# Optimization experiments

Measured on AMD Instinct MI355X. Metric: run time of the kernel, lower is better.

The kernel has to match this reference:

```python
import jax, jax.numpy as jnp
import numpy as np

B, S, QD = 1, 2048, 3072          # batch, seq, query_dim
H, D = 24, 128                    # heads, head_dim
INNER = H * D                     # 3072
MLP = 4 * QD                      # mlp_hidden_dim = 12288
EPS = 1e-5


def setup_inputs() -> dict:
    key = jax.random.key(0)
    k0, k1, k2 = jax.random.split(key, 3)
    hidden_states = jax.random.normal(k0, (B, S, QD), dtype=jnp.float32)
    # RoPE tables (non-neox / interleaved), [S, D/2]
    pos = jnp.arange(S, dtype=jnp.float32)
    inv_freq = 1.0 / (10000.0 ** (jnp.arange(0, D, 2, dtype=jnp.float32) / D))
    ang = pos[:, None] * inv_freq[None, :]
    cos, sin = jnp.cos(ang), jnp.sin(ang)
    # learned params
    W_qkv_mlp = jax.random.normal(k1, (QD, 3 * INNER + 2 * MLP), dtype=jnp.float32) * 0.02
    norm_q_w = jnp.ones((D,), dtype=jnp.float32)
    norm_k_w = jnp.ones((D,), dtype=jnp.float32)
    W_out = jax.random.normal(k2, (INNER + MLP, QD), dtype=jnp.float32) * 0.02
    b_out = jnp.zeros((QD,), dtype=jnp.float32)
    return {"hidden_states": hidden_states, "cos": cos, "sin": sin,
            "W_qkv_mlp": W_qkv_mlp, "norm_q_w": norm_q_w, "norm_k_w": norm_k_w,
            "W_out": W_out, "b_out": b_out}


def _rmsnorm(x, w, eps):
    return x * jax.lax.rsqrt(jnp.mean(x * x, axis=-1, keepdims=True) + eps) * w


def _rope_interleaved(x, cos, sin):
    # x: [B,S,H,D]; cos/sin: [S,D/2]; non-neox pairing (x[2i], x[2i+1]); fp32 math
    xf = x.astype(jnp.float32)
    x1, x2 = xf[..., 0::2], xf[..., 1::2]
    c = cos[None, :, None, :]
    s = sin[None, :, None, :]
    r1 = x1 * c - x2 * s
    r2 = x2 * c + x1 * s
    out = jnp.stack([r1, r2], axis=-1).reshape(x.shape)
    return out.astype(x.dtype)


def reference(hidden_states, cos, sin, W_qkv_mlp, norm_q_w, norm_k_w, W_out, b_out):
    # fused QKV + MLP input projection (no bias)
    h = hidden_states @ W_qkv_mlp                       # [B,S,3*INNER+2*MLP]
    qkv, mlp_hidden = jnp.split(h, [3 * INNER], axis=-1)
    q, k, v = jnp.split(qkv, 3, axis=-1)
    q = q.reshape(B, S, H, D)
    k = k.reshape(B, S, H, D)
    v = v.reshape(B, S, H, D)
    # per-head RMSNorm on q/k
    q = _rmsnorm(q, norm_q_w, EPS)
    k = _rmsnorm(k, norm_k_w, EPS)
    # interleaved RoPE
    q = _rope_interleaved(q, cos, sin)
    k = _rope_interleaved(k, cos, sin)
    # non-causal attention, scale = 1/sqrt(head_dim)
    scale = 1.0 / np.sqrt(D).astype(np.float32)
    scores = jnp.einsum('bqhd,bkhd->bhqk', q, k) * scale
    probs = jax.nn.softmax(scores, axis=-1)
    attn_out = jnp.einsum('bhqk,bkhd->bqhd', probs, v).reshape(B, S, INNER)
    # SwiGLU on fused MLP hidden (gate fused into first GEMM)
    x1, x2 = jnp.split(mlp_hidden, 2, axis=-1)
    mlp_out = jax.nn.silu(x1) * x2                      # [B,S,MLP]
    # fused output projection (with bias)
    return jnp.concatenate([attn_out, mlp_out], axis=-1) @ W_out + b_out
```

## Files before the change

kernel.cpp:

```cpp
#include <hip/hip_runtime.h>

typedef unsigned short u16;
typedef unsigned int u32;
typedef __attribute__((ext_vector_type(8))) __bf16 bf16x8;
typedef __attribute__((ext_vector_type(4))) float f32x4;
typedef __attribute__((ext_vector_type(8))) u16 u16x8;
typedef __attribute__((ext_vector_type(4))) float fv4;

#define DEVI __device__ __forceinline__

DEVI float bf2f(u16 u) { union { u32 i; float f; } v; v.i = ((u32)u) << 16; return v.f; }
DEVI u16 f2bf(float f) {
  union { float f; u32 i; } v; v.f = f;
  u32 r = v.i + 0x7fffu + ((v.i >> 16) & 1u);
  return (u16)(r >> 16);
}

#define GLD16(src, dst)                                                        \
  __builtin_amdgcn_global_load_lds(                                            \
      (const __attribute__((address_space(1))) void*)(src),                    \
      (__attribute__((address_space(3))) void*)(dst), 16, 0, 0)

DEVI f32x4 mfma16(bf16x8 a, bf16x8 b, f32x4 c) {
  return __builtin_amdgcn_mfma_f32_16x16x32_bf16(a, b, c, 0, 0, 0);
}

constexpr int S_    = 2048;
constexpr int QD_   = 3072;
constexpr int H_    = 24;
constexpr int N1_   = 33792;
constexpr int K1_   = 3072;
constexpr int K2_   = 15360;
constexpr int N2_   = 3072;
constexpr int MLP_  = 12288;

__global__ void k_cvt(const float* __restrict__ in, u16* __restrict__ out) {
  int i = blockIdx.x * blockDim.x + threadIdx.x;
  const fv4* p = (const fv4*)in + (size_t)i * 2;
  fv4 a = p[0], b = p[1];
  u16x8 r;
#pragma unroll
  for (int e = 0; e < 4; ++e) { r[e] = f2bf(a[e]); r[4 + e] = f2bf(b[e]); }
  ((u16x8*)out)[i] = r;
}

__global__ __launch_bounds__(256)
void k_tconv8(const float* __restrict__ in, u16* __restrict__ out,
              int R, int C) {
  const int t = threadIdx.x;
  const int R8 = t & 15, C8 = t >> 4;
  const int r0 = blockIdx.y * 128, c0 = blockIdx.x * 128;
  const float* src = in + (size_t)(r0 + R8 * 8) * C + c0 + C8 * 8;
  float rf[8][8];
#pragma unroll
  for (int r = 0; r < 8; ++r) {
    fv4 a = *(const fv4*)(src + (size_t)r * C);
    fv4 b = *(const fv4*)(src + (size_t)r * C + 4);
#pragma unroll
    for (int e = 0; e < 4; ++e) { rf[r][e] = a[e]; rf[r][4 + e] = b[e]; }
  }
  u16* dst = out + (size_t)(c0 + C8 * 8) * R + r0 + R8 * 8;
#pragma unroll
  for (int i = 0; i < 8; ++i) {
    u16x8 v;
#pragma unroll
    for (int j = 0; j < 8; ++j) v[j] = f2bf(rf[j][i]);
    *(u16x8*)(dst + (size_t)i * R) = v;
  }
}

template <int BM, int BN, int WM, int WN, bool OUTF32>
__global__ __launch_bounds__(256)
void k_gemm(const u16* __restrict__ A, const u16* __restrict__ Bt,
            void* __restrict__ Cout, const float* __restrict__ bias,
            int M, int N, int K) {
  constexpr int FM = WM / 16, FN = WN / 16;
  constexpr int WNC = BN / WN;
  __shared__ u16 As[BM * 32];
  __shared__ u16 Bs[BN * 32];
  const int t = threadIdx.x, w = t >> 6, lane = t & 63;
  const int m0 = blockIdx.x * BM, n0 = blockIdx.y * BN;
  const int wr = w / WNC, wc = w % WNC;
  const int g = lane >> 4, rr = lane & 15;
  const int sm = lane >> 2, sk = (lane & 3) * 8;
  f32x4 acc[FM][FN] = {};
  const int nk = K >> 5;
  for (int kt = 0; kt < nk; ++kt) {
    __syncthreads();
    const int kb = kt * 32 + sk;
#pragma unroll
    for (int c = 0; c < BM / 64; ++c) {
      const int ch = w + c * 4;
      GLD16(A + (size_t)(m0 + ch * 16 + sm) * K + kb, &As[ch * 512]);
    }
#pragma unroll
    for (int c = 0; c < BN / 64; ++c) {
      const int ch = w + c * 4;
      GLD16(Bt + (size_t)(n0 + ch * 16 + sm) * K + kb, &Bs[ch * 512]);
    }
    __syncthreads();
    bf16x8 af[FM], bfr[FN];
#pragma unroll
    for (int mi = 0; mi < FM; ++mi)
      af[mi] = *reinterpret_cast<const bf16x8*>(&As[(wr * WM + mi * 16 + rr) * 32 + g * 8]);
#pragma unroll
    for (int ni = 0; ni < FN; ++ni)
      bfr[ni] = *reinterpret_cast<const bf16x8*>(&Bs[(wc * WN + ni * 16 + rr) * 32 + g * 8]);
#pragma unroll
    for (int mi = 0; mi < FM; ++mi)
#pragma unroll
      for (int ni = 0; ni < FN; ++ni)
        acc[mi][ni] = mfma16(af[mi], bfr[ni], acc[mi][ni]);
  }
#pragma unroll
  for (int mi = 0; mi < FM; ++mi)
#pragma unroll
    for (int ni = 0; ni < FN; ++ni) {
      const int row = m0 + wr * WM + mi * 16 + g * 4;
      const int col = n0 + wc * WN + ni * 16 + rr;
#pragma unroll
      for (int j = 0; j < 4; ++j) {
        if constexpr (OUTF32)
          ((float*)Cout)[(size_t)(row + j) * N + col] = acc[mi][ni][j] + bias[col];
        else
          ((u16*)Cout)[(size_t)(row + j) * N + col] = f2bf(acc[mi][ni][j]);
      }
    }
}

#define BARX() asm volatile("s_barrier" ::: "memory")
#define LGKM0() asm volatile("s_waitcnt lgkmcnt(0)" ::: "memory")
__global__ __launch_bounds__(512, 2)
void k_gemm256(const u16* __restrict__ A, const u16* __restrict__ Bt,
               u16* __restrict__ C, int N, int K, int nbm) {
  extern __shared__ char smem[];
  const int t = threadIdx.x;
  const int w = t >> 6, lane = t & 63;
  const int wr = w >> 2, wc = w & 3, bh = wc >> 1;
  const int g = lane >> 4, rr = lane & 15;
  const int nwg = gridDim.x, bid = blockIdx.x;
  const int swz = (bid & 7) * (nwg >> 3) + (bid >> 3);
  const int m0 = (swz % nbm) * 256;
  const int n0 = (swz / nbm) * 256;
  const int o = t * 16;
  const int ou = o ^ (((o >> 9) & 1) << 5);
  const int srow = ((ou >> 10) >> 1) * 16 + ((ou >> 6) & 15);
  const int scol = ((ou >> 10) & 1) * 32 + ((ou & 63) >> 1);
  const int soff = (rr * 64 + g * 16) ^ (((rr >> 3) & 1) << 5);
  const int bnoff = (wc & 1) * 8192;
  const int nk = K >> 6;

  const u16* Arow = A + (size_t)(m0 + srow) * K + scol;
  const u16* Brow = Bt + (size_t)(n0 + srow) * K + scol;
#define LDSA(buf, h) (smem + ((buf) * 2 + (h)) * 16384 + w * 1024)
#define LDSB(buf, h) (smem + 65536 + ((buf) * 2 + (h)) * 16384 + w * 1024)
#define STG(rowptr, h, k0, dst)                                   \
  do {                                                            \
    const u16* _s = (rowptr) + (size_t)(h) * 128 * K + (k0);      \
    GLD16(_s, (dst));                                             \
    GLD16(_s + (size_t)64 * K, (dst) + 8192);                     \
  } while (0)

  STG(Arow, 0, 0, LDSA(0, 0));
  STG(Arow, 1, 0, LDSA(0, 1));
  STG(Brow, 0, 0, LDSB(0, 0));
  STG(Brow, 1, 0, LDSB(0, 1));
  STG(Brow, 0, 64, LDSB(1, 0));
  STG(Brow, 1, 64, LDSB(1, 1));
  STG(Arow, 0, 64, LDSA(1, 0));
  asm volatile("s_waitcnt vmcnt(6)" ::: "memory");
  BARX();

  f32x4 acc[8][4] = {};
  for (int j = 0; j < nk; ++j) {
    const int b = j & 1;
    const char* Ab = smem + ((b << 1) + wr) * 16384;
    const char* Bb = smem + 65536 + ((b << 1) + bh) * 16384;
    const int jb = (j + 2 < nk) ? j + 2 : nk - 1;
    bf16x8 aL[4][2], aH[4][2], bL[2][2], bH[2][2];
#pragma unroll
    for (int m = 0; m < 4; ++m)
#pragma unroll
      for (int kk = 0; kk < 2; ++kk)
        aL[m][kk] = *(const bf16x8*)(Ab + m * 2048 + kk * 1024 + soff);
#pragma unroll
    for (int n = 0; n < 2; ++n)
#pragma unroll
      for (int kk = 0; kk < 2; ++kk)
        bL[n][kk] = *(const bf16x8*)(Bb + bnoff + n * 2048 + kk * 1024 + soff);
    if (j + 1 < nk) STG(Arow, 1, (j + 1) * 64, LDSA((j + 1) & 1, 1));
    asm volatile("s_waitcnt lgkmcnt(8)" ::: "memory");
    BARX();
    LGKM0();
    __builtin_amdgcn_s_setprio(1);
#pragma unroll
    for (int m = 0; m < 4; ++m)
#pragma unroll
      for (int n = 0; n < 2; ++n)
#pragma unroll
        for (int kk = 0; kk < 2; ++kk)
          acc[m][n] = mfma16(aL[m][kk], bL[n][kk], acc[m][n]);
    __builtin_amdgcn_s_setprio(0);
    BARX();
#pragma unroll
    for (int n = 0; n < 2; ++n)
#pragma unroll
      for (int kk = 0; kk < 2; ++kk)
        bH[n][kk] = *(const bf16x8*)(Bb + bnoff + (n + 2) * 2048 + kk * 1024 + soff);
    BARX();
    LGKM0();
    __builtin_amdgcn_s_setprio(1);
#pragma unroll
    for (int m = 0; m < 4; ++m)
#pragma unroll
      for (int n = 0; n < 2; ++n)
#pragma unroll
        for (int kk = 0; kk < 2; ++kk)
          acc[m][n + 2] = mfma16(aL[m][kk], bH[n][kk], acc[m][n + 2]);
    __builtin_amdgcn_s_setprio(0);
    BARX();
#pragma unroll
    for (int m = 0; m < 4; ++m)
#pragma unroll
      for (int kk = 0; kk < 2; ++kk)
        aH[m][kk] = *(const bf16x8*)(Ab + (m + 4) * 2048 + kk * 1024 + soff);
    STG(Brow, 0, jb * 64, LDSB(b, 0));
    BARX();
    LGKM0();
    __builtin_amdgcn_s_setprio(1);
#pragma unroll
    for (int m = 0; m < 4; ++m)
#pragma unroll
      for (int n = 0; n < 2; ++n)
#pragma unroll
        for (int kk = 0; kk < 2; ++kk)
          acc[m + 4][n] = mfma16(aH[m][kk], bL[n][kk], acc[m + 4][n]);
    __builtin_amdgcn_s_setprio(0);
    BARX();
    STG(Brow, 1, jb * 64, LDSB(b, 1));
    STG(Arow, 0, jb * 64, LDSA(b, 0));
    asm volatile("s_waitcnt vmcnt(6)" ::: "memory");
    BARX();
    LGKM0();
    __builtin_amdgcn_s_setprio(1);
#pragma unroll
    for (int m = 0; m < 4; ++m)
#pragma unroll
      for (int n = 0; n < 2; ++n)
#pragma unroll
        for (int kk = 0; kk < 2; ++kk)
          acc[m + 4][n + 2] = mfma16(aH[m][kk], bH[n][kk], acc[m + 4][n + 2]);
    __builtin_amdgcn_s_setprio(0);
    BARX();
  }
#pragma unroll
  for (int m = 0; m < 8; ++m)
#pragma unroll
    for (int n = 0; n < 4; ++n) {
      const int row = m0 + wr * 128 + m * 16 + g * 4;
      const int col = n0 + wc * 64 + n * 16 + rr;
#pragma unroll
      for (int jj = 0; jj < 4; ++jj)
        C[(size_t)(row + jj) * N + col] = f2bf(acc[m][n][jj]);
    }
#undef LDSA
#undef LDSB
#undef STG
}

__global__ __launch_bounds__(256)
void k_qknr(u16* __restrict__ h, const float* __restrict__ cosT,
            const float* __restrict__ sinT, const float* __restrict__ wq,
            const float* __restrict__ wk) {
  const int row = blockIdx.x * 4 + (threadIdx.x >> 6);
  const int lane = threadIdx.x & 63;
  const int s = row / 48;
  const int r2 = row - s * 48;
  const int qk = r2 / 24;
  const int head = r2 - qk * 24;
  u16* base = h + (size_t)s * N1_ + qk * 3072 + head * 128;
  u32 pv = *(const u32*)(base + 2 * lane);
  float x1 = bf2f((u16)(pv & 0xffff)), x2 = bf2f((u16)(pv >> 16));
  float ss = x1 * x1 + x2 * x2;
#pragma unroll
  for (int off = 32; off >= 1; off >>= 1) ss += __shfl_xor(ss, off);
  const float inv = rsqrtf(ss * (1.0f / 128.0f) + 1e-5f);
  const float* wv = qk ? wk : wq;
  const float w1 = wv[2 * lane], w2 = wv[2 * lane + 1];
  const float c = cosT[s * 64 + lane], sn = sinT[s * 64 + lane];
  float xn1 = x1 * inv * w1, xn2 = x2 * inv * w2;
  float r1 = xn1 * c - xn2 * sn;
  float r2v = xn2 * c + xn1 * sn;
  if (!qk) { r1 *= 0.08838834764831845f; r2v *= 0.08838834764831845f; }
  *(u32*)(base + 2 * lane) = (u32)f2bf(r1) | ((u32)f2bf(r2v) << 16);
}

__global__ __launch_bounds__(256)
void k_vt(const u16* __restrict__ h, u16* __restrict__ vt) {
  __shared__ u16 tile[64][144];
  const int t = threadIdx.x;
  const int head = blockIdx.y;
  const int s0 = blockIdx.x * 64;
  {
    const int sl = t >> 2, cc = t & 3;
    const u16* src = h + (size_t)(s0 + sl) * N1_ + 6144 + head * 128 + cc * 32;
#pragma unroll
    for (int q = 0; q < 4; ++q)
      *(u16x8*)&tile[sl][cc * 32 + q * 8] = *(const u16x8*)(src + q * 8);
  }
  __syncthreads();
  {
    const int d = t & 127, half = t >> 7;
    u16* dst = vt + ((size_t)head * 128 + d) * S_ + s0 + half * 32;
#pragma unroll
    for (int q = 0; q < 4; ++q) {
      u16x8 v;
#pragma unroll
      for (int e = 0; e < 8; ++e) v[e] = tile[half * 32 + q * 8 + e][d];
      *(u16x8*)(dst + q * 8) = v;
    }
  }
}

__global__ __launch_bounds__(256)
void k_attn(const u16* __restrict__ h, const u16* __restrict__ vt,
            u16* __restrict__ cc) {
  extern __shared__ char smem[];
  char* KsB = smem;
  char* VsB = smem + 32768;
  const int t = threadIdx.x, w = t >> 6, lane = t & 63;
  const int g = lane >> 4, c = lane & 15;
  u16* Pw = (u16*)(smem + 65536 + w * 2304);
  const int head = blockIdx.y;
  const int q0 = blockIdx.x * 64 + w * 16;
  const int wb = w * 1024;

  const u16* ksrc[4];
  const u16* vsrc[4];
#pragma unroll
  for (int p = 0; p < 4; ++p) {
    const int o = p * 4096 + wb + lane * 16;
    {
      const int kc = o >> 12, r = (o >> 6) & 63, db = o & 63;
      ksrc[p] = h + (size_t)r * N1_ + 3072 + head * 128 + kc * 32 + db / 2;
    }
    {
      const int ks = o >> 13, d = (o >> 6) & 127, db = o & 63;
      vsrc[p] = vt + (size_t)(head * 128 + d) * S_ + ks * 32 + db / 2;
    }
  }
#define STAGEA(ts, buf)                                                     \
  do {                                                                      \
    const size_t _ka = (size_t)(ts) * 64 * N1_;                             \
    const int _kv = (ts) * 64;                                              \
    _Pragma("unroll") for (int p = 0; p < 4; ++p)                           \
        GLD16(ksrc[p] + _ka, KsB + (buf) * 16384 + p * 4096 + wb);          \
    _Pragma("unroll") for (int p = 0; p < 4; ++p)                           \
        GLD16(vsrc[p] + _kv, VsB + (buf) * 16384 + p * 4096 + wb);          \
  } while (0)

  bf16x8 aq[4];
  {
    const u16* qr = h + (size_t)(q0 + c) * N1_ + head * 128;
#pragma unroll
    for (int kc = 0; kc < 4; ++kc)
      aq[kc] = *reinterpret_cast<const bf16x8*>(qr + kc * 32 + g * 8);
  }
  f32x4 o[8] = {};
  float m_[4] = {-1e30f, -1e30f, -1e30f, -1e30f};
  float l_[4] = {0.f, 0.f, 0.f, 0.f};

  STAGEA(0, 0);
  STAGEA(1, 1);
  asm volatile("s_waitcnt vmcnt(8)" ::: "memory");
  __builtin_amdgcn_s_barrier();

  for (int tt = 0; tt < 32; ++tt) {
    const int buf = tt & 1;
    const char* Kb = KsB + buf * 16384;
    const char* Vb = VsB + buf * 16384;
    f32x4 sc[4] = {};
    __builtin_amdgcn_s_setprio(1);
#pragma unroll
    for (int nf = 0; nf < 4; ++nf)
#pragma unroll
      for (int kc = 0; kc < 4; ++kc) {
        bf16x8 bk = *(const bf16x8*)(Kb + kc * 4096 + (nf * 16 + c) * 64 + g * 16);
        sc[nf] = mfma16(aq[kc], bk, sc[nf]);
      }
    __builtin_amdgcn_s_setprio(0);
    float rmax[4];
#pragma unroll
    for (int j = 0; j < 4; ++j)
      rmax[j] = fmaxf(fmaxf(sc[0][j], sc[1][j]), fmaxf(sc[2][j], sc[3][j]));
#pragma unroll
    for (int j = 0; j < 4; ++j)
#pragma unroll
      for (int off = 8; off >= 1; off >>= 1)
        rmax[j] = fmaxf(rmax[j], __shfl_xor(rmax[j], off));
    float al[4], rs[4];
#pragma unroll
    for (int j = 0; j < 4; ++j) {
      const float mn = fmaxf(m_[j], rmax[j]);
      al[j] = __expf(m_[j] - mn);
      m_[j] = mn;
      rs[j] = 0.f;
    }
#pragma unroll
    for (int nf = 0; nf < 4; ++nf)
#pragma unroll
      for (int j = 0; j < 4; ++j) {
        const float pr = __expf(sc[nf][j] - m_[j]);
        sc[nf][j] = pr;
        rs[j] += pr;
      }
#pragma unroll
    for (int j = 0; j < 4; ++j) {
#pragma unroll
      for (int off = 8; off >= 1; off >>= 1) rs[j] += __shfl_xor(rs[j], off);
      l_[j] = l_[j] * al[j] + rs[j];
    }
#pragma unroll
    for (int of = 0; of < 8; ++of)
#pragma unroll
      for (int j = 0; j < 4; ++j) o[of][j] *= al[j];
#pragma unroll
    for (int nf = 0; nf < 4; ++nf)
#pragma unroll
      for (int j = 0; j < 4; ++j)
        Pw[(g * 4 + j) * 72 + nf * 16 + c] = f2bf(sc[nf][j]);
    asm volatile("s_waitcnt lgkmcnt(0)" ::: "memory");
    bf16x8 ap[2];
#pragma unroll
    for (int ks = 0; ks < 2; ++ks)
      ap[ks] = *(const bf16x8*)(Pw + c * 72 + ks * 32 + g * 8);
    __builtin_amdgcn_s_setprio(1);
#pragma unroll
    for (int of = 0; of < 8; ++of)
#pragma unroll
      for (int ks = 0; ks < 2; ++ks) {
        bf16x8 bv = *(const bf16x8*)(Vb + ks * 8192 + (of * 16 + c) * 64 + g * 16);
        o[of] = mfma16(ap[ks], bv, o[of]);
      }
    __builtin_amdgcn_s_setprio(0);
    __builtin_amdgcn_s_barrier();
    const int tn = (tt + 2 < 32) ? tt + 2 : 31;
    STAGEA(tn, buf);
    asm volatile("s_waitcnt vmcnt(8)" ::: "memory");
    __builtin_amdgcn_s_barrier();
  }
  float inv[4];
#pragma unroll
  for (int j = 0; j < 4; ++j) inv[j] = 1.0f / l_[j];
#pragma unroll
  for (int of = 0; of < 8; ++of)
#pragma unroll
    for (int j = 0; j < 4; ++j)
      cc[(size_t)(q0 + g * 4 + j) * K2_ + head * 128 + of * 16 + c] =
          f2bf(o[of][j] * inv[j]);
#undef STAGEA
}

__global__ void k_mlpact(const u16* __restrict__ h, u16* __restrict__ cc) {
  const int i = blockIdx.x * blockDim.x + threadIdx.x;
  const int s = i / 1536;
  const int j8 = i - s * 1536;
  const u16x8 a8 = *((const u16x8*)(h + (size_t)s * N1_ + 9216) + j8);
  const u16x8 b8 = *((const u16x8*)(h + (size_t)s * N1_ + 21504) + j8);
  u16x8 r;
#pragma unroll
  for (int e = 0; e < 8; ++e) {
    float a = bf2f(a8[e]), b = bf2f(b8[e]);
    float sv = a / (1.0f + expf(-a));
    r[e] = f2bf(sv * b);
  }
  *((u16x8*)(cc + (size_t)s * K2_ + 3072) + j8) = r;
}

extern "C" void kernel_launch(void* const* d_in, const int* in_sizes, int n_in,
                              void* d_out, int out_size, void* d_ws,
                              size_t ws_size, hipStream_t stream) {
  const float* hs   = (const float*)d_in[0];
  const float* cosT = (const float*)d_in[1];
  const float* sinT = (const float*)d_in[2];
  const float* W1   = (const float*)d_in[3];
  const float* wq   = (const float*)d_in[4];
  const float* wk   = (const float*)d_in[5];
  const float* W2   = (const float*)d_in[6];
  const float* bo   = (const float*)d_in[7];
  float* out = (float*)d_out;

  char* p = (char*)d_ws;
  u16* Abf  = (u16*)p; p += (size_t)S_ * K1_ * 2;
  u16* W1t  = (u16*)p; p += (size_t)N1_ * K1_ * 2;
  u16* W2t  = (u16*)p; p += (size_t)N2_ * K2_ * 2;
  u16* Hbuf = (u16*)p; p += (size_t)S_ * N1_ * 2;
  u16* Vt   = (u16*)p; p += (size_t)H_ * 128 * S_ * 2;
  u16* CC   = (u16*)p; p += (size_t)S_ * K2_ * 2;
  if ((size_t)(p - (char*)d_ws) > ws_size) return;

  k_cvt<<<(S_ * K1_) / (256 * 8), 256, 0, stream>>>(hs, Abf);
  k_tconv8<<<dim3(N1_ / 128, K1_ / 128), 256, 0, stream>>>(W1, W1t, K1_, N1_);
  k_tconv8<<<dim3(N2_ / 128, K2_ / 128), 256, 0, stream>>>(W2, W2t, K2_, N2_);

  hipError_t aerr = hipFuncSetAttribute(
      reinterpret_cast<const void*>(k_gemm256),
      hipFuncAttributeMaxDynamicSharedMemorySize, 131072);
  if (aerr == hipSuccess) {
    k_gemm256<<<dim3(1056), 512, 131072, stream>>>(Abf, W1t, Hbuf,
                                                   N1_, K1_, 8);
  } else {
    k_gemm<128, 128, 64, 64, false>
        <<<dim3(S_ / 128, N1_ / 128), 256, 0, stream>>>(Abf, W1t, Hbuf, nullptr,
                                                        S_, N1_, K1_);
  }
  k_qknr<<<(S_ * 2 * H_) / 4, 256, 0, stream>>>(Hbuf, cosT, sinT, wq, wk);
  k_vt<<<dim3(S_ / 64, H_), 256, 0, stream>>>(Hbuf, Vt);
  (void)hipFuncSetAttribute(reinterpret_cast<const void*>(k_attn),
                            hipFuncAttributeMaxDynamicSharedMemorySize, 75776);
  k_attn<<<dim3(S_ / 64, H_), 256, 75776, stream>>>(Hbuf, Vt, CC);
  k_mlpact<<<(S_ * MLP_) / (256 * 8), 256, 0, stream>>>(Hbuf, CC);
  k_gemm<128, 128, 64, 64, true>
      <<<dim3(S_ / 128, N2_ / 128), 256, 0, stream>>>(CC, W2t, out, bo,
                                                      S_, N2_, K2_);
}
```

Before: 1.238 ms.

## Split-K output projection on 256-tile GEMM with bf16 partials and reduce

The output projection GEMM (K=15360, N=3072) now runs on the larger 256x256 pipelined GEMM kernel with an 8-way split over K, so 768 workgroups are launched instead of 384 with 128x128 tiles. Each split writes bf16 partial tiles into the no-longer-needed W1t buffer, and a new reduction kernel sums the 8 partials and adds the bias in fp32. This is meant to fill the GPU better and use the faster GEMM kernel. In exchange it adds partial-sum traffic and an extra launch, and the partials are rounded to bf16 before summation, which costs some accuracy.

```diff
diff --git a/kernel.cpp b/kernel.cpp
--- a/kernel.cpp
+++ b/kernel.cpp
@@ -132,7 +132,7 @@
 #define LGKM0() asm volatile("s_waitcnt lgkmcnt(0)" ::: "memory")
 __global__ __launch_bounds__(512, 2)
 void k_gemm256(const u16* __restrict__ A, const u16* __restrict__ Bt,
-               u16* __restrict__ C, int N, int K, int nbm) {
+               u16* __restrict__ C, int N, int K, int nbm, int zmul, int nkt) {
   extern __shared__ char smem[];
   const int t = threadIdx.x;
   const int w = t >> 6, lane = t & 63;
@@ -140,18 +140,22 @@
   const int g = lane >> 4, rr = lane & 15;
   const int nwg = gridDim.x, bid = blockIdx.x;
   const int swz = (bid & 7) * (nwg >> 3) + (bid >> 3);
-  const int m0 = (swz % nbm) * 256;
-  const int n0 = (swz / nbm) * 256;
+  const int zz = swz / zmul;
+  const int rem = swz - zz * zmul;
+  const int m0 = (rem % nbm) * 256;
+  const int n0 = (rem / nbm) * 256;
+  const int koff = zz * nkt * 64;
   const int o = t * 16;
   const int ou = o ^ (((o >> 9) & 1) << 5);
   const int srow = ((ou >> 10) >> 1) * 16 + ((ou >> 6) & 15);
   const int scol = ((ou >> 10) & 1) * 32 + ((ou & 63) >> 1);
   const int soff = (rr * 64 + g * 16) ^ (((rr >> 3) & 1) << 5);
   const int bnoff = (wc & 1) * 8192;
-  const int nk = K >> 6;
-
-  const u16* Arow = A + (size_t)(m0 + srow) * K + scol;
-  const u16* Brow = Bt + (size_t)(n0 + srow) * K + scol;
+  const int nk = nkt;
+
+  const u16* Arow = A + (size_t)(m0 + srow) * K + koff + scol;
+  const u16* Brow = Bt + (size_t)(n0 + srow) * K + koff + scol;
+  u16* Cz = C + (size_t)zz * ((size_t)nbm * 256) * N;
 #define LDSA(buf, h) (smem + ((buf) * 2 + (h)) * 16384 + w * 1024)
 #define LDSB(buf, h) (smem + 65536 + ((buf) * 2 + (h)) * 16384 + w * 1024)
 #define STG(rowptr, h, k0, dst)                                   \
@@ -261,11 +265,31 @@
       const int col = n0 + wc * 64 + n * 16 + rr;
 #pragma unroll
       for (int jj = 0; jj < 4; ++jj)
-        C[(size_t)(row + jj) * N + col] = f2bf(acc[m][n][jj]);
+        Cz[(size_t)(row + jj) * N + col] = f2bf(acc[m][n][jj]);
     }
 #undef LDSA
 #undef LDSB
 #undef STG
+}
+
+__global__ __launch_bounds__(256)
+void k_red8(const u16* __restrict__ pc, const float* __restrict__ bias,
+            float* __restrict__ out) {
+  const size_t base = ((size_t)blockIdx.x * 256 + threadIdx.x) * 8;
+  float a[8] = {};
+#pragma unroll
+  for (int z = 0; z < 8; ++z) {
+    u16x8 v = *(const u16x8*)(pc + (size_t)z * (2048u * 3072u) + base);
+#pragma unroll
+    for (int e = 0; e < 8; ++e) a[e] += bf2f(v[e]);
+  }
+  const int col = (int)(base % 3072);
+  fv4 b0 = *(const fv4*)(bias + col), b1 = *(const fv4*)(bias + col + 4);
+  fv4 o0, o1;
+#pragma unroll
+  for (int e = 0; e < 4; ++e) { o0[e] = a[e] + b0[e]; o1[e] = a[4 + e] + b1[e]; }
+  *(fv4*)(out + base) = o0;
+  *(fv4*)(out + base + 4) = o1;
 }
 
 __global__ __launch_bounds__(256)
@@ -498,6 +522,7 @@
   u16* Vt   = (u16*)p; p += (size_t)H_ * 128 * S_ * 2;
   u16* CC   = (u16*)p; p += (size_t)S_ * K2_ * 2;
   if ((size_t)(p - (char*)d_ws) > ws_size) return;
+  u16* PC = W1t;
 
   k_cvt<<<(S_ * K1_) / (256 * 8), 256, 0, stream>>>(hs, Abf);
   k_tconv8<<<dim3(N1_ / 128, K1_ / 128), 256, 0, stream>>>(W1, W1t, K1_, N1_);
@@ -508,7 +533,7 @@
       hipFuncAttributeMaxDynamicSharedMemorySize, 131072);
   if (aerr == hipSuccess) {
     k_gemm256<<<dim3(1056), 512, 131072, stream>>>(Abf, W1t, Hbuf,
-                                                   N1_, K1_, 8);
+                                                   N1_, K1_, 8, 1056, 48);
   } else {
     k_gemm<128, 128, 64, 64, false>
         <<<dim3(S_ / 128, N1_ / 128), 256, 0, stream>>>(Abf, W1t, Hbuf, nullptr,
@@ -520,7 +545,13 @@
                             hipFuncAttributeMaxDynamicSharedMemorySize, 75776);
   k_attn<<<dim3(S_ / 64, H_), 256, 75776, stream>>>(Hbuf, Vt, CC);
   k_mlpact<<<(S_ * MLP_) / (256 * 8), 256, 0, stream>>>(Hbuf, CC);
-  k_gemm<128, 128, 64, 64, true>
-      <<<dim3(S_ / 128, N2_ / 128), 256, 0, stream>>>(CC, W2t, out, bo,
-                                                      S_, N2_, K2_);
-}
+  if (aerr == hipSuccess) {
+    k_gemm256<<<dim3(768), 512, 131072, stream>>>(CC, W2t, PC,
+                                                  N2_, K2_, 8, 96, 30);
+    k_red8<<<dim3((S_ * N2_) / (256 * 8)), 256, 0, stream>>>(PC, bo, out);
+  } else {
+    k_gemm<128, 128, 64, 64, true>
+        <<<dim3(S_ / 128, N2_ / 128), 256, 0, stream>>>(CC, W2t, out, bo,
+                                                        S_, N2_, K2_);
+  }
+}
```

New measurement: 1.019 ms. -17.7%, faster.
